# Kernel tuning notes

Hardware: AMD Instinct MI355X
Metric: run time of the kernel (lower is better)

The kernel has to match this reference:

```python
import jax, jax.numpy as jnp
import numpy as np

ALPHA = 1.0
MIN_FEATURE_SIZE = 1.0
SC = 1e-12                      # stabilizer added to first derivatives
EPS_V_FLOOR = 1e-32 / 6.0       # torch.tensor(1e-32 ** 1 / 6) == 1e-32/6 (** binds tighter than /)


def _grad2d(phi, d):
    """Vectorized equivalent of numerical_gradient_2d: central differences in the
    interior, one-sided forward/backward differences at the boundaries."""
    gx = jnp.concatenate([
        (phi[1:2, :] - phi[0:1, :]) / d,           # forward diff at i == 0
        (phi[2:, :] - phi[:-2, :]) / (2.0 * d),    # central diff in interior
        (phi[-1:, :] - phi[-2:-1, :]) / d,         # backward diff at i == H-1
    ], axis=0)
    gy = jnp.concatenate([
        (phi[:, 1:2] - phi[:, 0:1]) / d,
        (phi[:, 2:] - phi[:, :-2]) / (2.0 * d),
        (phi[:, -1:] - phi[:, -2:-1]) / d,
    ], axis=1)
    return gx, gy


def setup_inputs() -> dict:
    key = jax.random.key(0)
    eps = jax.random.normal(key, (4096, 4096), dtype=jnp.float32)
    grid_size = jnp.asarray(0.05, dtype=jnp.float32)
    return {"eps": eps, "grid_size": grid_size}


def reference(eps, grid_size):
    # mirror the field along axis 1 (torch.cat((eps, eps.flip(1)), dim=1)) -> [H, 2W]
    eps = jnp.concatenate([eps, eps[:, ::-1]], axis=1)

    # ls_derivatives: first derivatives (+SC), then second derivatives of those
    eps_x, eps_y = _grad2d(eps, grid_size)
    eps_x = eps_x + SC
    eps_y = eps_y + SC
    eps_xx, eps_xy = _grad2d(eps_x, grid_size)
    _, eps_yy = _grad2d(eps_y, grid_size)

    pi_d = np.pi / (1.1 * MIN_FEATURE_SIZE)
    eps_v = jnp.maximum(jnp.sqrt(eps_x**2 + eps_y**2), EPS_V_FLOOR)
    k = (eps_x**2 * eps_yy - 2.0 * eps_x * eps_y * eps_xy + eps_y**2 * eps_xx) / eps_v**3
    curve_const = jnp.abs(k * jnp.arctan(eps_v / eps)) - pi_d
    return jnp.nansum(ALPHA * jnp.maximum(curve_const, 0.0) * grid_size**2)
```

## Files before the change

### kernel.cpp

```cpp
#include <hip/hip_runtime.h>
#include <math.h>


#define BLOCK_X 256
#define ROWS_PER 16

__device__ __forceinline__ float fast_atan_ratio(float v, float c, float rv)
{
    const float rc = __builtin_amdgcn_rcpf(c);
    const float q  = v * rc;
    const float iq = c * rv;
    const bool  big = fabsf(q) > 1.0f;
    const float t  = big ? iq : q;
    const float s  = t * t;
    float p = fmaf(s, -0.01172120f, 0.05265332f);
    p = fmaf(s, p, -0.11643287f);
    p = fmaf(s, p,  0.19354346f);
    p = fmaf(s, p, -0.33262347f);
    p = fmaf(s, p,  0.99997726f);
    const float at = p * t;
    const float hp = copysignf(1.57079632679f, q);
    return big ? (hp - at) : at;
}

template<bool INT>
__device__ __forceinline__ float compute_rows(
    const float* __restrict__ eps, int Hn, int Wn, int i0,
    int j, int jm, int jmm, int cjp, int cjpp,
    float rd, float syj, float sym, float syp)
{
    const float rd2 = 0.5f * rd;
    const float SC = 1e-12f;
    const float FLOORV = (float)(1e-32 / 6.0);
    const float pi_d = 3.14159265358979323846f / 1.1f;

    float acc = 0.0f;
    for (int r = 0; r < ROWS_PER; ++r) {
        const int i = i0 + r;
        int im, ip, imm, ipp;
        float sxi, sxm, sxp;
        if (INT) {
            im = i - 1; ip = i + 1; imm = i - 2; ipp = i + 2;
            sxi = rd2; sxm = rd2; sxp = rd2;
        } else {
            im  = (i > 0) ? i - 1 : 0;
            ip  = (i < Hn - 1) ? i + 1 : Hn - 1;
            imm = (im > 0) ? im - 1 : 0;
            ipp = (ip < Hn - 1) ? ip + 1 : Hn - 1;
            sxi = (i == 0 || i == Hn - 1) ? rd : rd2;
            sxm = (im == 0) ? rd : rd2;
            sxp = (ip == Hn - 1) ? rd : rd2;
        }

        const float* rowc  = eps + (size_t)i   * (size_t)Wn;
        const float* rown  = eps + (size_t)im  * (size_t)Wn;
        const float* rows_ = eps + (size_t)ip  * (size_t)Wn;
        const float* rownn = eps + (size_t)imm * (size_t)Wn;
        const float* rowss = eps + (size_t)ipp * (size_t)Wn;

        const float e_c  = rowc[j];
        const float e_n  = rown[j],   e_s  = rows_[j];
        const float e_nn = rownn[j],  e_ss = rowss[j];
        const float e_w  = rowc[jm],  e_e  = rowc[cjp];
        const float e_ww = rowc[jmm], e_ee = rowc[cjpp];
        const float e_nw = rown[jm],  e_ne = rown[cjp];
        const float e_sw = rows_[jm], e_se = rows_[cjp];

        const float ex = fmaf(e_s - e_n, sxi, SC);
        const float ey = fmaf(e_e - e_w, syj, SC);

        float exn = fmaf(e_c - e_nn, sxm, SC);
        float exs = fmaf(e_ss - e_c, sxp, SC);
        if (!INT) {
            if (i == 0)      exn = ex;
            if (i == Hn - 1) exs = ex;
        }
        const float exx = (exs - exn) * sxi;

        float eyw = fmaf(e_c - e_ww, sym, SC);
        const float eye = fmaf(e_ee - e_c, syp, SC);
        if (j == 0) eyw = ey;
        const float eyy = (eye - eyw) * syj;

        const float exy = ((e_se - e_ne) - (e_sw - e_nw)) * (sxi * syj);

        const float t1 = ex * ex;
        const float t2 = ey * ey;
        float num = t1 * eyy;
        num = fmaf(t2, exx, num);
        num = fmaf(-2.0f * (ex * ey), exy, num);

        float ev = __builtin_amdgcn_sqrtf(t1 + t2);
        ev = fmaxf(ev, FLOORV);
        const float rv = __builtin_amdgcn_rcpf(ev);
        const float k  = num * (rv * rv) * rv;
        const float at = fast_atan_ratio(ev, e_c, rv);
        const float cc = fabsf(k * at) - pi_d;
        acc += fmaxf(cc, 0.0f);
    }
    return acc;
}

__global__ __launch_bounds__(BLOCK_X) void curve_partial_kernel(
    const float* __restrict__ eps, const float* __restrict__ gs,
    double* __restrict__ partial, int Hn, int Wn)
{
    const int tx = threadIdx.x;
    const int j  = blockIdx.x * BLOCK_X + tx;
    const int i0 = blockIdx.y * ROWS_PER;
    const float d  = gs[0];
    const float rd = 1.0f / d;
    const float rd2 = 0.5f * rd;

    float accf = 0.0f;
    {
        const int jm  = (j > 0) ? j - 1 : 0;
        const int jmm = (j > 1) ? j - 2 : 0;
        const int jp = j + 1, jpp = j + 2;
        const int cjp  = (jp  < Wn) ? jp  : (2 * Wn - 1 - jp);
        const int cjpp = (jpp < Wn) ? jpp : (2 * Wn - 1 - jpp);
        const float syj = (j == 0)  ? rd : rd2;
        const float sym = (jm == 0) ? rd : rd2;
        const float syp = rd2;

        const bool interior = (i0 >= 2) && (i0 + ROWS_PER + 1 < Hn);
        if (interior)
            accf = compute_rows<true >(eps, Hn, Wn, i0, j, jm, jmm, cjp, cjpp, rd, syj, sym, syp);
        else
            accf = compute_rows<false>(eps, Hn, Wn, i0, j, jm, jmm, cjp, cjpp, rd, syj, sym, syp);
    }

    double acc = (double)accf;
    #pragma unroll
    for (int off = 32; off > 0; off >>= 1)
        acc += __shfl_down(acc, off, 64);
    __shared__ double lds[BLOCK_X / 64];
    const int lane = tx & 63, wv = tx >> 6;
    if (lane == 0) lds[wv] = acc;
    __syncthreads();
    if (tx == 0) {
        partial[blockIdx.y * gridDim.x + blockIdx.x] =
            lds[0] + lds[1] + lds[2] + lds[3];
    }
}

__global__ __launch_bounds__(256) void curve_finish_kernel(
    const double* __restrict__ partial, int n,
    const float* __restrict__ gs, float* __restrict__ out)
{
    const int tx = threadIdx.x;
    double acc = 0.0;
    for (int idx = tx; idx < n; idx += 256) acc += partial[idx];
    #pragma unroll
    for (int off = 32; off > 0; off >>= 1)
        acc += __shfl_down(acc, off, 64);
    __shared__ double lds[4];
    const int lane = tx & 63, wv = tx >> 6;
    if (lane == 0) lds[wv] = acc;
    __syncthreads();
    if (tx == 0) {
        const double d = (double)gs[0];
        out[0] = (float)((lds[0] + lds[1] + lds[2] + lds[3]) * 2.0 * d * d);
    }
}

extern "C" void kernel_launch(void* const* d_in, const int* in_sizes, int n_in,
                              void* d_out, int out_size, void* d_ws, size_t ws_size,
                              hipStream_t stream) {
    const float* eps = (const float*)d_in[0];
    const float* gs  = (const float*)d_in[1];
    float* out = (float*)d_out;

    const int n = in_sizes[0];
    int Wn = (int)(sqrt((double)n) + 0.5);
    int Hn = n / Wn;

    const int gx = (Wn + BLOCK_X - 1) / BLOCK_X;
    const int gy = (Hn + ROWS_PER - 1) / ROWS_PER;
    double* partial = (double*)d_ws;

    curve_partial_kernel<<<dim3(gx, gy), BLOCK_X, 0, stream>>>(eps, gs, partial, Hn, Wn);
    curve_finish_kernel<<<1, 256, 0, stream>>>(partial, gx * gy, gs, out);
}
```

Measured before the change: 120.1 us.

## Process four columns per thread with float4 loads and register stencil reuse

Each thread now computes a 4-wide column strip, loading each stencil row as a float4 plus small halo loads, so neighbouring column values are reused from registers instead of being reloaded per output. Rows per block drop from 16 to 8, and launch bounds add a min-blocks hint. Edge column strips fall back to a scalar per-column path that handles the mirror boundary. The aim is fewer, wider memory instructions and fewer redundant loads. The costs are higher register pressure and fewer threads in the grid.

```diff
diff --git a/kernel.cpp b/kernel.cpp
--- a/kernel.cpp
+++ b/kernel.cpp
@@ -3,7 +3,8 @@
 
 
 #define BLOCK_X 256
-#define ROWS_PER 16
+#define ROWS_PER 8
+#define COLS_PER 4
 
 __device__ __forceinline__ float fast_atan_ratio(float v, float c, float rv)
 {
@@ -24,10 +25,8 @@
 }
 
 template<bool INT>
-__device__ __forceinline__ float compute_rows(
-    const float* __restrict__ eps, int Hn, int Wn, int i0,
-    int j, int jm, int jmm, int cjp, int cjpp,
-    float rd, float syj, float sym, float syp)
+__device__ __forceinline__ float vec4_cols(
+    const float* __restrict__ eps, int Hn, int Wn, int i0, int j0, float rd)
 {
     const float rd2 = 0.5f * rd;
     const float SC = 1e-12f;
@@ -37,6 +36,7 @@
     float acc = 0.0f;
     for (int r = 0; r < ROWS_PER; ++r) {
         const int i = i0 + r;
+        if (!INT && i >= Hn) break;
         int im, ip, imm, ipp;
         float sxi, sxm, sxp;
         if (INT) {
@@ -51,6 +51,91 @@
             sxm = (im == 0) ? rd : rd2;
             sxp = (ip == Hn - 1) ? rd : rd2;
         }
+        const float* rc  = eps + (size_t)i   * (size_t)Wn;
+        const float* rm  = eps + (size_t)im  * (size_t)Wn;
+        const float* rp  = eps + (size_t)ip  * (size_t)Wn;
+        const float* rmm = eps + (size_t)imm * (size_t)Wn;
+        const float* rpp = eps + (size_t)ipp * (size_t)Wn;
+
+        const float4 aNN = *(const float4*)(rmm + j0);
+        const float4 aM  = *(const float4*)(rm  + j0);
+        const float4 aC  = *(const float4*)(rc  + j0);
+        const float4 aP  = *(const float4*)(rp  + j0);
+        const float4 aSS = *(const float4*)(rpp + j0);
+        const float2 cL  = *(const float2*)(rc + j0 - 2);
+        const float2 cR  = *(const float2*)(rc + j0 + 4);
+        const float mL = rm[j0 - 1], mR = rm[j0 + 4];
+        const float pL = rp[j0 - 1], pR = rp[j0 + 4];
+
+        const float C[8]  = {cL.x, cL.y, aC.x, aC.y, aC.z, aC.w, cR.x, cR.y};
+        const float M[6]  = {mL, aM.x, aM.y, aM.z, aM.w, mR};
+        const float P[6]  = {pL, aP.x, aP.y, aP.z, aP.w, pR};
+        const float NN[4] = {aNN.x, aNN.y, aNN.z, aNN.w};
+        const float SS[4] = {aSS.x, aSS.y, aSS.z, aSS.w};
+
+        #pragma unroll
+        for (int x = 0; x < 4; ++x) {
+            const float e_c = C[x + 2];
+            const float ex  = fmaf(P[x + 1] - M[x + 1], sxi, SC);
+            const float ey  = fmaf(C[x + 3] - C[x + 1], rd2, SC);
+            float exn = fmaf(e_c - NN[x], sxm, SC);
+            float exs = fmaf(SS[x] - e_c, sxp, SC);
+            if (!INT) {
+                if (i == 0)      exn = ex;
+                if (i == Hn - 1) exs = ex;
+            }
+            const float exx = (exs - exn) * sxi;
+            const float eyw = fmaf(e_c - C[x], rd2, SC);
+            const float eye = fmaf(C[x + 4] - e_c, rd2, SC);
+            const float eyy = (eye - eyw) * rd2;
+            const float exy = ((P[x + 2] - M[x + 2]) - (P[x] - M[x])) * (sxi * rd2);
+
+            const float t1 = ex * ex;
+            const float t2 = ey * ey;
+            float num = t1 * eyy;
+            num = fmaf(t2, exx, num);
+            num = fmaf(-2.0f * (ex * ey), exy, num);
+
+            float ev = __builtin_amdgcn_sqrtf(t1 + t2);
+            ev = fmaxf(ev, FLOORV);
+            const float rv = __builtin_amdgcn_rcpf(ev);
+            const float k  = num * (rv * rv) * rv;
+            const float at = fast_atan_ratio(ev, e_c, rv);
+            const float cc = fabsf(k * at) - pi_d;
+            acc += fmaxf(cc, 0.0f);
+        }
+    }
+    return acc;
+}
+
+__device__ float scalar_col(const float* __restrict__ eps, int Hn, int Wn,
+                            int i0, int j, float rd)
+{
+    const float rd2 = 0.5f * rd;
+    const float SC = 1e-12f;
+    const float FLOORV = (float)(1e-32 / 6.0);
+    const float pi_d = 3.14159265358979323846f / 1.1f;
+
+    const int jm  = (j > 0) ? j - 1 : 0;
+    const int jmm = (j > 1) ? j - 2 : 0;
+    const int jp = j + 1, jpp = j + 2;
+    const int cjp  = (jp  < Wn) ? jp  : (2 * Wn - 1 - jp);
+    const int cjpp = (jpp < Wn) ? jpp : (2 * Wn - 1 - jpp);
+    const float syj = (j == 0)  ? rd : rd2;
+    const float sym = (jm == 0) ? rd : rd2;
+    const float syp = rd2;
+
+    float acc = 0.0f;
+    for (int r = 0; r < ROWS_PER; ++r) {
+        const int i = i0 + r;
+        if (i >= Hn) break;
+        const int im  = (i > 0) ? i - 1 : 0;
+        const int ip  = (i < Hn - 1) ? i + 1 : Hn - 1;
+        const int imm = (im > 0) ? im - 1 : 0;
+        const int ipp = (ip < Hn - 1) ? ip + 1 : Hn - 1;
+        const float sxi = (i == 0 || i == Hn - 1) ? rd : rd2;
+        const float sxm = (im == 0) ? rd : rd2;
+        const float sxp = (ip == Hn - 1) ? rd : rd2;
 
         const float* rowc  = eps + (size_t)i   * (size_t)Wn;
         const float* rown  = eps + (size_t)im  * (size_t)Wn;
@@ -68,20 +153,15 @@
 
         const float ex = fmaf(e_s - e_n, sxi, SC);
         const float ey = fmaf(e_e - e_w, syj, SC);
-
         float exn = fmaf(e_c - e_nn, sxm, SC);
         float exs = fmaf(e_ss - e_c, sxp, SC);
-        if (!INT) {
-            if (i == 0)      exn = ex;
-            if (i == Hn - 1) exs = ex;
-        }
+        if (i == 0)      exn = ex;
+        if (i == Hn - 1) exs = ex;
         const float exx = (exs - exn) * sxi;
-
         float eyw = fmaf(e_c - e_ww, sym, SC);
         const float eye = fmaf(e_ee - e_c, syp, SC);
         if (j == 0) eyw = ey;
         const float eyy = (eye - eyw) * syj;
-
         const float exy = ((e_se - e_ne) - (e_sw - e_nw)) * (sxi * syj);
 
         const float t1 = ex * ex;
@@ -101,33 +181,26 @@
     return acc;
 }
 
-__global__ __launch_bounds__(BLOCK_X) void curve_partial_kernel(
+__global__ __launch_bounds__(BLOCK_X, 4) void curve_partial_kernel(
     const float* __restrict__ eps, const float* __restrict__ gs,
     double* __restrict__ partial, int Hn, int Wn)
 {
     const int tx = threadIdx.x;
-    const int j  = blockIdx.x * BLOCK_X + tx;
+    const int j0 = (blockIdx.x * BLOCK_X + tx) * COLS_PER;
     const int i0 = blockIdx.y * ROWS_PER;
-    const float d  = gs[0];
-    const float rd = 1.0f / d;
-    const float rd2 = 0.5f * rd;
+    const float rd = 1.0f / gs[0];
 
     float accf = 0.0f;
-    {
-        const int jm  = (j > 0) ? j - 1 : 0;
-        const int jmm = (j > 1) ? j - 2 : 0;
-        const int jp = j + 1, jpp = j + 2;
-        const int cjp  = (jp  < Wn) ? jp  : (2 * Wn - 1 - jp);
-        const int cjpp = (jpp < Wn) ? jpp : (2 * Wn - 1 - jpp);
-        const float syj = (j == 0)  ? rd : rd2;
-        const float sym = (jm == 0) ? rd : rd2;
-        const float syp = rd2;
-
-        const bool interior = (i0 >= 2) && (i0 + ROWS_PER + 1 < Hn);
-        if (interior)
-            accf = compute_rows<true >(eps, Hn, Wn, i0, j, jm, jmm, cjp, cjpp, rd, syj, sym, syp);
-        else
-            accf = compute_rows<false>(eps, Hn, Wn, i0, j, jm, jmm, cjp, cjpp, rd, syj, sym, syp);
+    if (j0 < Wn) {
+        const bool iint = (i0 >= 2) && (i0 + ROWS_PER + 1 < Hn);
+        const bool jint = (j0 >= 4) && (j0 + 8 <= Wn);
+        if (jint) {
+            accf = iint ? vec4_cols<true >(eps, Hn, Wn, i0, j0, rd)
+                        : vec4_cols<false>(eps, Hn, Wn, i0, j0, rd);
+        } else {
+            for (int c = 0; c < COLS_PER; ++c)
+                if (j0 + c < Wn) accf += scalar_col(eps, Hn, Wn, i0, j0 + c, rd);
+        }
     }
 
     double acc = (double)accf;
@@ -175,7 +248,7 @@
     int Wn = (int)(sqrt((double)n) + 0.5);
     int Hn = n / Wn;
 
-    const int gx = (Wn + BLOCK_X - 1) / BLOCK_X;
+    const int gx = (Wn + BLOCK_X * COLS_PER - 1) / (BLOCK_X * COLS_PER);
     const int gy = (Hn + ROWS_PER - 1) / ROWS_PER;
     double* partial = (double*)d_ws;
 
```

After: 127.4 us. +6.1%, slower.

## Stage stencil tile in LDS with float2 loads and two columns per thread

Applied to the files above, without the earlier changes.

Interior blocks now load a (ROWS_PER+4) x (2*BLOCK_X+4) halo tile of the input into shared memory with vectorized float2 loads, then compute the curvature stencil from LDS, two output columns per thread. The curvature formula is reorganized algebraically so the SC stabilizer and grid-spacing factors drop out, and rsq replaces sqrt+rcp. Edge blocks fall back to a generic global-memory path. This cuts redundant global loads of the 13-point stencil, at the cost of LDS traffic, a barrier, and dropping SC/floor handling that could change results in degenerate cases.

```diff
diff --git a/kernel.cpp b/kernel.cpp
--- a/kernel.cpp
+++ b/kernel.cpp
@@ -3,54 +3,78 @@
 
 
 #define BLOCK_X 256
-#define ROWS_PER 16
-
-__device__ __forceinline__ float fast_atan_ratio(float v, float c, float rv)
-{
-    const float rc = __builtin_amdgcn_rcpf(c);
-    const float q  = v * rc;
-    const float iq = c * rv;
-    const bool  big = fabsf(q) > 1.0f;
-    const float t  = big ? iq : q;
-    const float s  = t * t;
-    float p = fmaf(s, -0.01172120f, 0.05265332f);
-    p = fmaf(s, p, -0.11643287f);
-    p = fmaf(s, p,  0.19354346f);
-    p = fmaf(s, p, -0.33262347f);
-    p = fmaf(s, p,  0.99997726f);
-    const float at = p * t;
-    const float hp = copysignf(1.57079632679f, q);
-    return big ? (hp - at) : at;
-}
-
-template<bool INT>
-__device__ __forceinline__ float compute_rows(
-    const float* __restrict__ eps, int Hn, int Wn, int i0,
-    int j, int jm, int jmm, int cjp, int cjpp,
-    float rd, float syj, float sym, float syp)
+#define ROWS_PER 8
+#define TILE_COLS (2 * BLOCK_X + 4)
+#define TILE_F2   (TILE_COLS / 2)
+#define TILE_H    (ROWS_PER + 4)
+
+__device__ __forceinline__ float curve_pt(
+    float nn, float nw, float n, float ne,
+    float ww, float w, float c, float e, float ee,
+    float sw, float s, float se, float ss,
+    float rd2, float two_d)
+{
+    const float pi_d = 3.14159265358979323846f / 1.1f;
+    const float u  = s - n;
+    const float v  = e - w;
+    const float U  = fmaf(-2.0f, c, ss + nn);
+    const float V  = fmaf(-2.0f, c, ee + ww);
+    const float X2 = 2.0f * ((se - ne) - (sw - nw));
+    const float u2 = u * u, v2 = v * v, uv = u * v;
+    float W = u2 * V;
+    W = fmaf(v2, U, W);
+    W = fmaf(-uv, X2, W);
+    const float S  = u2 + v2;
+    const float rsq = __builtin_amdgcn_rsqf(S);
+    const float r3  = (rsq * rsq) * rsq;
+    const float kk  = fabsf(W) * r3;
+    const float ae  = fabsf(c);
+    const float rc  = __builtin_amdgcn_rcpf(ae);
+    const float sq  = S * rsq;
+    const float q   = (rd2 * sq) * rc;
+    const float iq  = (ae * rsq) * two_d;
+    const bool  big = q > 1.0f;
+    const float t   = big ? iq : q;
+    const float s2  = t * t;
+    float p = fmaf(s2, -0.01172120f, 0.05265332f);
+    p = fmaf(s2, p, -0.11643287f);
+    p = fmaf(s2, p,  0.19354346f);
+    p = fmaf(s2, p, -0.33262347f);
+    p = fmaf(s2, p,  0.99997726f);
+    float at = p * t;
+    at = big ? (1.57079632679f - at) : at;
+    const float cc = fmaf(kk * rd2, at, -pi_d);
+    return fmaxf(cc, 0.0f);
+}
+
+__device__ float generic_rows(const float* __restrict__ eps, int Hn, int Wn,
+                              int i0, int j, float rd)
 {
     const float rd2 = 0.5f * rd;
     const float SC = 1e-12f;
     const float FLOORV = (float)(1e-32 / 6.0);
     const float pi_d = 3.14159265358979323846f / 1.1f;
 
+    const int jm  = (j > 0) ? j - 1 : 0;
+    const int jmm = (j > 1) ? j - 2 : 0;
+    const int jp = j + 1, jpp = j + 2;
+    const int cjp  = (jp  < Wn) ? jp  : (2 * Wn - 1 - jp);
+    const int cjpp = (jpp < Wn) ? jpp : (2 * Wn - 1 - jpp);
+    const float syj = (j == 0)  ? rd : rd2;
+    const float sym = (jm == 0) ? rd : rd2;
+    const float syp = rd2;
+
     float acc = 0.0f;
     for (int r = 0; r < ROWS_PER; ++r) {
         const int i = i0 + r;
-        int im, ip, imm, ipp;
-        float sxi, sxm, sxp;
-        if (INT) {
-            im = i - 1; ip = i + 1; imm = i - 2; ipp = i + 2;
-            sxi = rd2; sxm = rd2; sxp = rd2;
-        } else {
-            im  = (i > 0) ? i - 1 : 0;
-            ip  = (i < Hn - 1) ? i + 1 : Hn - 1;
-            imm = (im > 0) ? im - 1 : 0;
-            ipp = (ip < Hn - 1) ? ip + 1 : Hn - 1;
-            sxi = (i == 0 || i == Hn - 1) ? rd : rd2;
-            sxm = (im == 0) ? rd : rd2;
-            sxp = (ip == Hn - 1) ? rd : rd2;
-        }
+        if (i >= Hn) break;
+        const int im  = (i > 0) ? i - 1 : 0;
+        const int ip  = (i < Hn - 1) ? i + 1 : Hn - 1;
+        const int imm = (im > 0) ? im - 1 : 0;
+        const int ipp = (ip < Hn - 1) ? ip + 1 : Hn - 1;
+        const float sxi = (i == 0 || i == Hn - 1) ? rd : rd2;
+        const float sxm = (im == 0) ? rd : rd2;
+        const float sxp = (ip == Hn - 1) ? rd : rd2;
 
         const float* rowc  = eps + (size_t)i   * (size_t)Wn;
         const float* rown  = eps + (size_t)im  * (size_t)Wn;
@@ -68,20 +92,15 @@
 
         const float ex = fmaf(e_s - e_n, sxi, SC);
         const float ey = fmaf(e_e - e_w, syj, SC);
-
         float exn = fmaf(e_c - e_nn, sxm, SC);
         float exs = fmaf(e_ss - e_c, sxp, SC);
-        if (!INT) {
-            if (i == 0)      exn = ex;
-            if (i == Hn - 1) exs = ex;
-        }
+        if (i == 0)      exn = ex;
+        if (i == Hn - 1) exs = ex;
         const float exx = (exs - exn) * sxi;
-
         float eyw = fmaf(e_c - e_ww, sym, SC);
         const float eye = fmaf(e_ee - e_c, syp, SC);
         if (j == 0) eyw = ey;
         const float eyy = (eye - eyw) * syj;
-
         const float exy = ((e_se - e_ne) - (e_sw - e_nw)) * (sxi * syj);
 
         const float t1 = ex * ex;
@@ -94,53 +113,125 @@
         ev = fmaxf(ev, FLOORV);
         const float rv = __builtin_amdgcn_rcpf(ev);
         const float k  = num * (rv * rv) * rv;
-        const float at = fast_atan_ratio(ev, e_c, rv);
-        const float cc = fabsf(k * at) - pi_d;
+        const float ae = fabsf(e_c);
+        const float rc = __builtin_amdgcn_rcpf(ae);
+        const float q  = ev * rc;
+        const float iq = ae * rv;
+        const bool  big = q > 1.0f;
+        const float t  = big ? iq : q;
+        const float s2 = t * t;
+        float p = fmaf(s2, -0.01172120f, 0.05265332f);
+        p = fmaf(s2, p, -0.11643287f);
+        p = fmaf(s2, p,  0.19354346f);
+        p = fmaf(s2, p, -0.33262347f);
+        p = fmaf(s2, p,  0.99997726f);
+        float at = p * t;
+        at = big ? (1.57079632679f - at) : at;
+        const float cc = fabsf(k) * at - pi_d;
         acc += fmaxf(cc, 0.0f);
     }
     return acc;
 }
 
-__global__ __launch_bounds__(BLOCK_X) void curve_partial_kernel(
+__global__ __launch_bounds__(BLOCK_X, 4) void curve_partial_kernel(
     const float* __restrict__ eps, const float* __restrict__ gs,
     double* __restrict__ partial, int Hn, int Wn)
 {
+    __shared__ float2 tile2[TILE_H * TILE_F2];
     const int tx = threadIdx.x;
-    const int j  = blockIdx.x * BLOCK_X + tx;
+    const int jb = blockIdx.x * (2 * BLOCK_X);
     const int i0 = blockIdx.y * ROWS_PER;
     const float d  = gs[0];
     const float rd = 1.0f / d;
     const float rd2 = 0.5f * rd;
+    const float two_d = 2.0f * d;
+
+    const int p0 = jb + 2 * tx;
+    const int p1 = p0 + 1;
+
+    const bool row_int = (i0 >= 2) && (i0 + ROWS_PER + 2 <= Hn);
 
     float accf = 0.0f;
-    {
-        const int jm  = (j > 0) ? j - 1 : 0;
-        const int jmm = (j > 1) ? j - 2 : 0;
-        const int jp = j + 1, jpp = j + 2;
-        const int cjp  = (jp  < Wn) ? jp  : (2 * Wn - 1 - jp);
-        const int cjpp = (jpp < Wn) ? jpp : (2 * Wn - 1 - jpp);
-        const float syj = (j == 0)  ? rd : rd2;
-        const float sym = (jm == 0) ? rd : rd2;
-        const float syp = rd2;
-
-        const bool interior = (i0 >= 2) && (i0 + ROWS_PER + 1 < Hn);
-        if (interior)
-            accf = compute_rows<true >(eps, Hn, Wn, i0, j, jm, jmm, cjp, cjpp, rd, syj, sym, syp);
-        else
-            accf = compute_rows<false>(eps, Hn, Wn, i0, j, jm, jmm, cjp, cjpp, rd, syj, sym, syp);
+    if (row_int) {
+        const float* gbase = eps + (size_t)(i0 - 2) * (size_t)Wn;
+        const bool cint = (jb >= 2) && (jb + 2 * BLOCK_X + 2 <= Wn);
+        if (cint) {
+            const float2* g2 = (const float2*)(gbase + (jb - 2));
+            const size_t rs = (size_t)(Wn / 2);
+            #pragma unroll
+            for (int r = 0; r < TILE_H; ++r)
+                tile2[r * TILE_F2 + tx] = g2[(size_t)r * rs + tx];
+            if (tx < 2) {
+                #pragma unroll
+                for (int r = 0; r < TILE_H; ++r)
+                    tile2[r * TILE_F2 + BLOCK_X + tx] = g2[(size_t)r * rs + BLOCK_X + tx];
+            }
+        } else {
+            float* tf = (float*)tile2;
+            int c0 = jb - 2 + 2 * tx, c1 = c0 + 1;
+            c0 = (c0 < 0) ? 0 : ((c0 >= Wn) ? 2 * Wn - 1 - c0 : c0);
+            c1 = (c1 < 0) ? 0 : ((c1 >= Wn) ? 2 * Wn - 1 - c1 : c1);
+            #pragma unroll
+            for (int r = 0; r < TILE_H; ++r) {
+                tf[r * TILE_COLS + 2 * tx]     = gbase[(size_t)r * Wn + c0];
+                tf[r * TILE_COLS + 2 * tx + 1] = gbase[(size_t)r * Wn + c1];
+            }
+            if (tx < 2) {
+                int e0 = jb - 2 + 2 * (BLOCK_X + tx), e1 = e0 + 1;
+                e0 = (e0 < 0) ? 0 : ((e0 >= Wn) ? 2 * Wn - 1 - e0 : e0);
+                e1 = (e1 < 0) ? 0 : ((e1 >= Wn) ? 2 * Wn - 1 - e1 : e1);
+                #pragma unroll
+                for (int r = 0; r < TILE_H; ++r) {
+                    tf[r * TILE_COLS + 2 * (BLOCK_X + tx)]     = gbase[(size_t)r * Wn + e0];
+                    tf[r * TILE_COLS + 2 * (BLOCK_X + tx) + 1] = gbase[(size_t)r * Wn + e1];
+                }
+            }
+        }
+        __syncthreads();
+
+        if (p0 >= 2 && p1 < Wn) {
+            const float2* t2 = tile2;
+            const int b = tx;
+            #pragma unroll
+            for (int r = 0; r < ROWS_PER; ++r) {
+                const float2 A  = t2[(r + 0) * TILE_F2 + b + 1];
+                const float2 B0 = t2[(r + 1) * TILE_F2 + b    ];
+                const float2 B1 = t2[(r + 1) * TILE_F2 + b + 1];
+                const float2 B2 = t2[(r + 1) * TILE_F2 + b + 2];
+                const float2 C0 = t2[(r + 2) * TILE_F2 + b    ];
+                const float2 C1 = t2[(r + 2) * TILE_F2 + b + 1];
+                const float2 C2 = t2[(r + 2) * TILE_F2 + b + 2];
+                const float2 D0 = t2[(r + 3) * TILE_F2 + b    ];
+                const float2 D1 = t2[(r + 3) * TILE_F2 + b + 1];
+                const float2 D2 = t2[(r + 3) * TILE_F2 + b + 2];
+                const float2 E  = t2[(r + 4) * TILE_F2 + b + 1];
+                accf += curve_pt(A.x, B0.y, B1.x, B1.y,
+                                 C0.x, C0.y, C1.x, C1.y, C2.x,
+                                 D0.y, D1.x, D1.y, E.x, rd2, two_d);
+                accf += curve_pt(A.y, B1.x, B1.y, B2.x,
+                                 C0.y, C1.x, C1.y, C2.x, C2.y,
+                                 D1.x, D1.y, D2.x, E.y, rd2, two_d);
+            }
+        } else {
+            if (p0 < Wn) accf += generic_rows(eps, Hn, Wn, i0, p0, rd);
+            if (p1 < Wn) accf += generic_rows(eps, Hn, Wn, i0, p1, rd);
+        }
+    } else {
+        if (p0 < Wn) accf += generic_rows(eps, Hn, Wn, i0, p0, rd);
+        if (p1 < Wn) accf += generic_rows(eps, Hn, Wn, i0, p1, rd);
     }
 
     double acc = (double)accf;
     #pragma unroll
     for (int off = 32; off > 0; off >>= 1)
         acc += __shfl_down(acc, off, 64);
-    __shared__ double lds[BLOCK_X / 64];
+    __shared__ double ldsr[BLOCK_X / 64];
     const int lane = tx & 63, wv = tx >> 6;
-    if (lane == 0) lds[wv] = acc;
+    if (lane == 0) ldsr[wv] = acc;
     __syncthreads();
     if (tx == 0) {
         partial[blockIdx.y * gridDim.x + blockIdx.x] =
-            lds[0] + lds[1] + lds[2] + lds[3];
+            ldsr[0] + ldsr[1] + ldsr[2] + ldsr[3];
     }
 }
 
@@ -175,7 +266,7 @@
     int Wn = (int)(sqrt((double)n) + 0.5);
     int Hn = n / Wn;
 
-    const int gx = (Wn + BLOCK_X - 1) / BLOCK_X;
+    const int gx = (Wn + 2 * BLOCK_X - 1) / (2 * BLOCK_X);
     const int gy = (Hn + ROWS_PER - 1) / ROWS_PER;
     double* partial = (double*)d_ws;
 
```

Measured after the change: 124.8 us. +4.0%, slower.
